# Performance work log

Measured on AMD Instinct MI355X. Metric: run time of the kernel, lower is better.

Reference implementation:

```python
import jax, jax.numpy as jnp
import numpy as np

D = 512      # d_model
H = 8        # num_heads
HD = D // H  # head_dim = 64
NI = 3       # num_inputs


def setup_inputs() -> dict:
    key = jax.random.key(0)
    ks = jax.random.split(key, 20)
    b, n, ni = 4, 8192, 4096
    s = 0.02
    inp = {
        "x": jax.random.normal(ks[0], (b, n, D), jnp.float32),
        "emb0": jax.random.normal(ks[1], (b, ni, D), jnp.float32),
        "emb1": jax.random.normal(ks[2], (b, ni, D), jnp.float32),
        "emb2": jax.random.normal(ks[3], (b, ni, D), jnp.float32),
        "Wq": jax.random.normal(ks[4], (D, D), jnp.float32) * s,
        "bq": jnp.zeros((D,), jnp.float32),
        "Wk": jax.random.normal(ks[5], (NI, D, D), jnp.float32) * s,
        "bk": jnp.zeros((NI, D), jnp.float32),
        "Wv": jax.random.normal(ks[6], (NI, D, D), jnp.float32) * s,
        "bv": jnp.zeros((NI, D), jnp.float32),
        "Wo": jax.random.normal(ks[7], (D, D), jnp.float32) * s,
        "bo": jnp.zeros((D,), jnp.float32),
        "mask0": jax.random.randint(ks[8], (b, ni), 0, 2).astype(bool),
        "mask1": jax.random.randint(ks[9], (b, ni), 0, 2).astype(bool),
        "mask2": jax.random.randint(ks[10], (b, ni), 0, 2).astype(bool),
    }
    return inp


def _heads(t, b):
    # [b, n, D] -> [b, H, n, HD]
    return t.reshape(b, -1, H, HD).transpose(0, 2, 1, 3)


def reference(x, emb0, emb1, emb2, Wq, bq, Wk, bk, Wv, bv, Wo, bo, mask0, mask1, mask2):
    b, n, _ = x.shape
    q = jax.nn.softmax(_heads(x @ Wq.T + bq, b), axis=-1)  # [b,H,n,HD]
    out = q
    for i, (emb, mask) in enumerate(((emb0, mask0), (emb1, mask1), (emb2, mask2))):
        k = jax.nn.softmax(_heads(emb @ Wk[i].T + bk[i], b), axis=-1)  # [b,H,ni,HD]
        v = _heads(emb @ Wv[i].T + bv[i], b)                            # [b,H,ni,HD]
        k = jnp.where(mask[:, None, :, None], k, 0.0)
        k_sum = k.sum(axis=2, keepdims=True)                            # [b,H,1,HD]
        d_inv = 1.0 / jnp.sum(q * k_sum, axis=-1, keepdims=True)        # [b,H,n,1]
        kv = jnp.einsum('bhsd,bhse->bhde', k, v)                        # [b,H,HD,HD]
        out = out + jnp.einsum('bhnd,bhde->bhne', q, kv) * d_inv
    out = out.transpose(0, 2, 1, 3).reshape(b, n, D) / NI
    return out @ Wo.T + bo
```

## Files before the change

kernel.cpp:

```cpp
#include <hip/hip_runtime.h>

#define D_MODEL 512
#define NH 8
#define HD_ 64
#define NUM_I 3
#define B_ 4
#define NSEQ 8192
#define SSEQ 4096

typedef __attribute__((ext_vector_type(8))) short short8;
typedef __attribute__((ext_vector_type(4))) float floatx4;

static constexpr size_t Q_OFF    = 0;
static constexpr size_t Q2_OFF   = 8388608;
static constexpr size_t KT_OFF   = 16777216;
static constexpr size_t VT_OFF   = 20971520;
static constexpr size_t WB_OFF   = 25165824;
static constexpr size_t KV_OFF   = 26214400;
static constexpr size_t KS_OFF   = 26607616;
static constexpr size_t KVB_OFF  = 26613760;
static constexpr size_t FLAG_OFF = 26712064;

__device__ __forceinline__ float bf2f(unsigned short u) {
    union { unsigned i; float f; } v; v.i = ((unsigned)u) << 16; return v.f;
}
__device__ __forceinline__ unsigned short f2bf(float f) {
    union { float f; unsigned i; } v; v.f = f;
    unsigned r = v.i + 0x7fffu + ((v.i >> 16) & 1u);
    return (unsigned short)(r >> 16);
}
__device__ __forceinline__ void gld16(const void* g, void* l) {
    __builtin_amdgcn_global_load_lds((const __attribute__((address_space(1))) void*)g,
                                     (__attribute__((address_space(3))) void*)l, 16, 0, 0);
}
__device__ __forceinline__ short8 cvt8(const float4& a, const float4& b) {
    short8 r;
    r[0] = (short)f2bf(a.x); r[1] = (short)f2bf(a.y);
    r[2] = (short)f2bf(a.z); r[3] = (short)f2bf(a.w);
    r[4] = (short)f2bf(b.x); r[5] = (short)f2bf(b.y);
    r[6] = (short)f2bf(b.z); r[7] = (short)f2bf(b.w);
    return r;
}

__global__ void mask_mode_kernel(const int* __restrict__ m, int* __restrict__ flag)
{
    __shared__ int any;
    if (threadIdx.x == 0) any = 0;
    __syncthreads();
    const unsigned v = (unsigned)m[threadIdx.x];
    if (v > 1u) atomicOr(&any, 1);
    __syncthreads();
    if (threadIdx.x == 0) *flag = any;
}

__global__ __launch_bounds__(256)
void f2bf_kernel(const float* __restrict__ in, unsigned short* __restrict__ out, int n8)
{
    const int i = blockIdx.x * 256 + threadIdx.x;
    if (i >= n8) return;
    const float4 a = ((const float4*)in)[2*i];
    const float4 b = ((const float4*)in)[2*i + 1];
    ((short8*)out)[i] = cvt8(a, b);
}

template<int EPI, int OUT, bool AFP32>
__global__ __launch_bounds__(256)
void proj2(const void* __restrict__ Av, const unsigned short* __restrict__ W,
           const float* __restrict__ bias, const int* __restrict__ mask,
           const int* __restrict__ maskmode, void* __restrict__ Cv)
{
    __shared__ short Ws[64 * 520];
    const int tid = threadIdx.x;
    const int wid = tid >> 6, lane = tid & 63;
    const int l15 = lane & 15, lq = lane >> 4;
    const int m0w = blockIdx.x * 256 + wid * 64;
    const int n0  = blockIdx.y * 64;

#pragma unroll
    for (int j = 0; j < 16; ++j) {
        const int row = wid * 16 + j;
        gld16(W + (size_t)(n0 + row) * D_MODEL + lane * 8, Ws + row * 520);
    }
    __syncthreads();

    floatx4 acc[4][4] = {};
    const float*          Af = (const float*)Av;
    const unsigned short* Ab = (const unsigned short*)Av;

    size_t abase[4];
#pragma unroll
    for (int mt = 0; mt < 4; ++mt)
        abase[mt] = (size_t)(m0w + mt * 16 + l15) * D_MODEL + lq * 8;

    short8 afc[4];
    if (AFP32) {
        float4 buf[2][4][2];
#pragma unroll
        for (int mt = 0; mt < 4; ++mt) {
            const float4* p0 = (const float4*)(Af + abase[mt]);
            buf[0][mt][0] = p0[0]; buf[0][mt][1] = p0[1];
            const float4* p1 = (const float4*)(Af + abase[mt] + 32);
            buf[1][mt][0] = p1[0]; buf[1][mt][1] = p1[1];
        }
#pragma unroll
        for (int mt = 0; mt < 4; ++mt) afc[mt] = cvt8(buf[0][mt][0], buf[0][mt][1]);
#pragma unroll
        for (int kk = 0; kk < 16; ++kk) {
            const int k0 = kk * 32;
            if (kk < 14) {
#pragma unroll
                for (int mt = 0; mt < 4; ++mt) {
                    const float4* p = (const float4*)(Af + abase[mt] + k0 + 64);
                    buf[kk & 1][mt][0] = p[0]; buf[kk & 1][mt][1] = p[1];
                }
            }
            short8 bfr[4];
#pragma unroll
            for (int nt = 0; nt < 4; ++nt)
                bfr[nt] = *(const short8*)&Ws[(nt * 16 + l15) * 520 + k0 + lq * 8];
#pragma unroll
            for (int mt = 0; mt < 4; ++mt)
#pragma unroll
                for (int nt = 0; nt < 4; ++nt)
                    acc[mt][nt] = __builtin_amdgcn_mfma_f32_16x16x32_bf16(afc[mt], bfr[nt], acc[mt][nt], 0, 0, 0);
            if (kk < 15) {
#pragma unroll
                for (int mt = 0; mt < 4; ++mt)
                    afc[mt] = cvt8(buf[(kk + 1) & 1][mt][0], buf[(kk + 1) & 1][mt][1]);
            }
        }
    } else {
        short8 buf[2][4];
#pragma unroll
        for (int mt = 0; mt < 4; ++mt) {
            buf[0][mt] = *(const short8*)(Ab + abase[mt]);
            buf[1][mt] = *(const short8*)(Ab + abase[mt] + 32);
        }
#pragma unroll
        for (int mt = 0; mt < 4; ++mt) afc[mt] = buf[0][mt];
#pragma unroll
        for (int kk = 0; kk < 16; ++kk) {
            const int k0 = kk * 32;
            if (kk < 14) {
#pragma unroll
                for (int mt = 0; mt < 4; ++mt)
                    buf[kk & 1][mt] = *(const short8*)(Ab + abase[mt] + k0 + 64);
            }
            short8 bfr[4];
#pragma unroll
            for (int nt = 0; nt < 4; ++nt)
                bfr[nt] = *(const short8*)&Ws[(nt * 16 + l15) * 520 + k0 + lq * 8];
#pragma unroll
            for (int mt = 0; mt < 4; ++mt)
#pragma unroll
                for (int nt = 0; nt < 4; ++nt)
                    acc[mt][nt] = __builtin_amdgcn_mfma_f32_16x16x32_bf16(afc[mt], bfr[nt], acc[mt][nt], 0, 0, 0);
            if (kk < 15) {
#pragma unroll
                for (int mt = 0; mt < 4; ++mt) afc[mt] = buf[(kk + 1) & 1][mt];
            }
        }
    }

    float bl[4];
#pragma unroll
    for (int nt = 0; nt < 4; ++nt) bl[nt] = bias[n0 + nt * 16 + l15];
#pragma unroll
    for (int mt = 0; mt < 4; ++mt)
#pragma unroll
        for (int nt = 0; nt < 4; ++nt)
#pragma unroll
            for (int r = 0; r < 4; ++r) acc[mt][nt][r] += bl[nt];

    if (EPI >= 1) {
#pragma unroll
        for (int mt = 0; mt < 4; ++mt)
#pragma unroll
            for (int r = 0; r < 4; ++r) {
                float mx = fmaxf(fmaxf(acc[mt][0][r], acc[mt][1][r]),
                                 fmaxf(acc[mt][2][r], acc[mt][3][r]));
#pragma unroll
                for (int off = 1; off < 16; off <<= 1) mx = fmaxf(mx, __shfl_xor(mx, off));
                float s = 0.f;
#pragma unroll
                for (int nt = 0; nt < 4; ++nt) {
                    const float e = __expf(acc[mt][nt][r] - mx);
                    acc[mt][nt][r] = e; s += e;
                }
#pragma unroll
                for (int off = 1; off < 16; off <<= 1) s += __shfl_xor(s, off);
                const float inv = 1.f / s;
#pragma unroll
                for (int nt = 0; nt < 4; ++nt) acc[mt][nt][r] *= inv;
            }
    }
    if (EPI == 2) {
        const int bytemode = *maskmode;
#pragma unroll
        for (int mt = 0; mt < 4; ++mt)
#pragma unroll
            for (int r = 0; r < 4; ++r) {
                const int grow = m0w + mt * 16 + lq * 4 + r;
                const bool keep = bytemode ? (((const unsigned char*)mask)[grow] != 0)
                                           : (mask[grow] != 0);
                if (!keep) {
#pragma unroll
                    for (int nt = 0; nt < 4; ++nt) acc[mt][nt][r] = 0.f;
                }
            }
    }

    if (OUT == 2) {
        __syncthreads();
        short* tw = Ws + wid * 4608;
#pragma unroll
        for (int mt = 0; mt < 4; ++mt)
#pragma unroll
            for (int nt = 0; nt < 4; ++nt) {
                ushort4 p;
                p.x = f2bf(acc[mt][nt][0]); p.y = f2bf(acc[mt][nt][1]);
                p.z = f2bf(acc[mt][nt][2]); p.w = f2bf(acc[mt][nt][3]);
                *(ushort4*)&tw[(nt * 16 + l15) * 72 + mt * 16 + lq * 4] = p;
            }
        __syncthreads();
        const int b_idx  = m0w >> 12;
        const int s_base = m0w & 4095;
        const int h = blockIdx.y;
        unsigned short* outp = (unsigned short*)Cv +
            ((size_t)(b_idx * NH + h) * 64 + lane) * SSEQ + s_base;
        const short* src = &tw[lane * 72];
#pragma unroll
        for (int sc = 0; sc < 8; ++sc)
            *(short8*)&outp[sc * 8] = *(const short8*)&src[sc * 8];
    } else {
#pragma unroll
        for (int mt = 0; mt < 4; ++mt)
#pragma unroll
            for (int r = 0; r < 4; ++r) {
                const size_t row = m0w + mt * 16 + lq * 4 + r;
#pragma unroll
                for (int nt = 0; nt < 4; ++nt) {
                    const int col = n0 + nt * 16 + l15;
                    if (OUT == 1)
                        ((unsigned short*)Cv)[row * D_MODEL + col] = f2bf(acc[mt][nt][r]);
                    else
                        ((float*)Cv)[row * D_MODEL + col] = acc[mt][nt][r];
                }
            }
    }
}

__global__ __launch_bounds__(256)
void kv_accum_mfma(const unsigned short* __restrict__ kT, const unsigned short* __restrict__ vT,
                   float* __restrict__ kv, float* __restrict__ ksum, int i_idx)
{
    const int chunk = blockIdx.x;
    const int h = blockIdx.y, b = blockIdx.z;
    __shared__ short As[2048];
    __shared__ short Bs[2048];
    const int tid = threadIdx.x;
    const int wid = tid >> 6, lane = tid & 63;
    const int wm  = wid & 1,  wn  = wid >> 1;
    const int l15 = lane & 15, lq = lane >> 4;

    const size_t base = (size_t)(b * NH + h) * 64 * SSEQ + chunk * 512;
    const int srow = tid & 63, ssub = tid >> 6;
    const unsigned short* Ag = vT + base + (size_t)srow * SSEQ + ssub * 8;
    const unsigned short* Bg = kT + base + (size_t)srow * SSEQ + ssub * 8;
    short* AsW = As + wid * 512;
    short* BsW = Bs + wid * 512;

    floatx4 acc[2][2] = {};
    floatx4 ks[2] = {};
    short8 ones;
#pragma unroll
    for (int j = 0; j < 8; ++j) ones[j] = (short)0x3F80;

    const int aoff = (wm*32 + l15)*8;
    const int boff = (wn*32 + l15)*8;

    for (int k0 = 0; k0 < 512; k0 += 32) {
        __syncthreads();
        gld16(Ag + k0, AsW);
        gld16(Bg + k0, BsW);
        __syncthreads();
        short8 af[2], bfr[2];
#pragma unroll
        for (int mt = 0; mt < 2; ++mt) af[mt]  = *(const short8*)&As[lq*512 + aoff + mt*128];
#pragma unroll
        for (int nt = 0; nt < 2; ++nt) bfr[nt] = *(const short8*)&Bs[lq*512 + boff + nt*128];
#pragma unroll
        for (int mt = 0; mt < 2; ++mt)
#pragma unroll
            for (int nt = 0; nt < 2; ++nt)
                acc[mt][nt] = __builtin_amdgcn_mfma_f32_16x16x32_bf16(af[mt], bfr[nt], acc[mt][nt], 0, 0, 0);
        if (wm == 0) {
#pragma unroll
            for (int nt = 0; nt < 2; ++nt)
                ks[nt] = __builtin_amdgcn_mfma_f32_16x16x32_bf16(ones, bfr[nt], ks[nt], 0, 0, 0);
        }
    }
    float* kvb = kv + (size_t)((i_idx*B_ + b)*NH + h) * 4096;
#pragma unroll
    for (int mt = 0; mt < 2; ++mt)
#pragma unroll
        for (int nt = 0; nt < 2; ++nt)
#pragma unroll
            for (int r = 0; r < 4; ++r) {
                const int e = wm*32 + mt*16 + lq*4 + r;
                const int d = wn*32 + nt*16 + l15;
                atomicAdd(&kvb[e*64 + d], acc[mt][nt][r]);
            }
    if (wm == 0 && lq == 0) {
        float* ksb = ksum + (size_t)((i_idx*B_ + b)*NH + h) * 64;
#pragma unroll
        for (int nt = 0; nt < 2; ++nt)
            atomicAdd(&ksb[wn*32 + nt*16 + l15], ks[nt][0]);
    }
}

__global__ __launch_bounds__(256)
void combine_mfma(const unsigned short* __restrict__ Q, const unsigned short* __restrict__ kvT,
                  const float* __restrict__ ksum, unsigned short* __restrict__ Qo)
{
    const int m0 = blockIdx.x * 128;
    const int h  = blockIdx.y;
    const int b  = m0 >> 13;
    __shared__ short qs[8192];
    __shared__ float skl[NUM_I][64];
    __shared__ float dinv[NUM_I][128];
    const int tid = threadIdx.x;
    const int wid = tid >> 6, lane = tid & 63;
    const int l15 = lane & 15, lq = lane >> 4;

    const unsigned short* Qbase = Q + (size_t)m0 * D_MODEL + h * 64;
#pragma unroll
    for (int j = 0; j < 4; ++j) {
        const int g = tid + j * 256;
        const int row = g & 127, c = g >> 7;
        gld16(Qbase + (size_t)row * D_MODEL + c * 8, qs + (size_t)(wid*64 + j*256) * 8);
    }
    if (tid < NUM_I * 64) {
        const int i = tid >> 6, d = tid & 63;
        skl[i][d] = ksum[(size_t)((i*B_ + b)*NH + h) * 64 + d];
    }
    __syncthreads();
    for (int it = tid; it < NUM_I * 128; it += 256) {
        const int i = it >> 7, row = it & 127;
        float s = 0.f;
#pragma unroll
        for (int d = 0; d < 64; ++d)
            s += bf2f((unsigned short)qs[(d >> 3)*1024 + row*8 + (d & 7)]) * skl[i][d];
        dinv[i][row] = 1.f / s;
    }
    __syncthreads();

    short8 af[2][2];
#pragma unroll
    for (int mt = 0; mt < 2; ++mt)
#pragma unroll
        for (int ks = 0; ks < 2; ++ks)
            af[mt][ks] = *(const short8*)&qs[(ks*4 + lq)*1024 + (wid*32 + mt*16 + l15)*8];

    floatx4 accO[2][4] = {};
    for (int i = 0; i < NUM_I; ++i) {
        const unsigned short* kvb = kvT + (size_t)((i*B_ + b)*NH + h) * 4096;
        short8 bfr[4][2];
#pragma unroll
        for (int nt = 0; nt < 4; ++nt)
#pragma unroll
            for (int ks = 0; ks < 2; ++ks)
                bfr[nt][ks] = *(const short8*)&kvb[(nt*16 + l15)*64 + ks*32 + lq*8];
#pragma unroll
        for (int mt = 0; mt < 2; ++mt)
#pragma unroll
            for (int nt = 0; nt < 4; ++nt) {
                floatx4 p = {};
                p = __builtin_amdgcn_mfma_f32_16x16x32_bf16(af[mt][0], bfr[nt][0], p, 0, 0, 0);
                p = __builtin_amdgcn_mfma_f32_16x16x32_bf16(af[mt][1], bfr[nt][1], p, 0, 0, 0);
#pragma unroll
                for (int r = 0; r < 4; ++r) {
                    const int row = wid*32 + mt*16 + lq*4 + r;
                    accO[mt][nt][r] += p[r] * dinv[i][row];
                }
            }
    }
    const float inv3 = 1.f / 3.f;
#pragma unroll
    for (int mt = 0; mt < 2; ++mt)
#pragma unroll
        for (int nt = 0; nt < 4; ++nt)
#pragma unroll
            for (int r = 0; r < 4; ++r) {
                const int row = wid*32 + mt*16 + lq*4 + r;
                const int col = nt*16 + l15;
                const float qv = bf2f((unsigned short)qs[(col >> 3)*1024 + row*8 + (col & 7)]);
                Qo[(size_t)(m0 + row) * D_MODEL + h*64 + col] = f2bf((qv + accO[mt][nt][r]) * inv3);
            }
}

extern "C" void kernel_launch(void* const* d_in, const int* in_sizes, int n_in,
                              void* d_out, int out_size, void* d_ws, size_t ws_size,
                              hipStream_t stream)
{
    const float* x      = (const float*)d_in[0];
    const float* emb[3] = {(const float*)d_in[1], (const float*)d_in[2], (const float*)d_in[3]};
    const float* Wq = (const float*)d_in[4];
    const float* bq = (const float*)d_in[5];
    const float* Wk = (const float*)d_in[6];
    const float* bk = (const float*)d_in[7];
    const float* Wv = (const float*)d_in[8];
    const float* bv = (const float*)d_in[9];
    const float* Wo = (const float*)d_in[10];
    const float* bo = (const float*)d_in[11];
    const int* mask[3] = {(const int*)d_in[12], (const int*)d_in[13], (const int*)d_in[14]};
    float* out = (float*)d_out;

    float* ws = (float*)d_ws;
    unsigned short* qb   = (unsigned short*)(ws + Q_OFF);
    unsigned short* q2b  = (unsigned short*)(ws + Q2_OFF);
    unsigned short* kT   = (unsigned short*)(ws + KT_OFF);
    unsigned short* vT   = (unsigned short*)(ws + VT_OFF);
    unsigned short* wb   = (unsigned short*)(ws + WB_OFF);
    unsigned short* wqb  = wb;
    unsigned short* wkb  = wb + 262144;
    unsigned short* wvb  = wb + 1048576;
    unsigned short* wob  = wb + 1835008;
    float* kv   = ws + KV_OFF;
    float* ksum = ws + KS_OFF;
    unsigned short* kvb16 = (unsigned short*)(ws + KVB_OFF);
    int*   flag = (int*)(ws + FLAG_OFF);

    mask_mode_kernel<<<1, 256, 0, stream>>>(mask[0], flag);
    hipMemsetAsync(kv, 0, (size_t)(NUM_I*B_*NH*HD_*HD_ + NUM_I*B_*NH*HD_) * sizeof(float), stream);

    f2bf_kernel<<<128, 256, 0, stream>>>(Wq, wqb, 32768);
    f2bf_kernel<<<384, 256, 0, stream>>>(Wk, wkb, 98304);
    f2bf_kernel<<<384, 256, 0, stream>>>(Wv, wvb, 98304);
    f2bf_kernel<<<128, 256, 0, stream>>>(Wo, wob, 32768);

    const dim3 gq(B_*NSEQ/256, NH);
    const dim3 gk(B_*SSEQ/256, NH);

    proj2<1, 1, true ><<<gq, 256, 0, stream>>>(x, wqb, bq, nullptr, nullptr, qb);
    for (int i = 0; i < NUM_I; ++i) {
        proj2<2, 2, true ><<<gk, 256, 0, stream>>>(emb[i], wkb + (size_t)i*262144,
                                                   bk + (size_t)i*D_MODEL, mask[i], flag, kT);
        proj2<0, 2, true ><<<gk, 256, 0, stream>>>(emb[i], wvb + (size_t)i*262144,
                                                   bv + (size_t)i*D_MODEL, nullptr, nullptr, vT);
        kv_accum_mfma<<<dim3(8, NH, B_), 256, 0, stream>>>(kT, vT, kv, ksum, i);
    }
    f2bf_kernel<<<192, 256, 0, stream>>>(kv, kvb16, 49152);
    combine_mfma<<<dim3(B_*NSEQ/128, NH), 256, 0, stream>>>(qb, kvb16, ksum, q2b);
    proj2<0, 0, false><<<gq, 256, 0, stream>>>(q2b, wob, bo, nullptr, nullptr, out);
}
```

Before: 679.7 us.

## Pre-convert activations to bf16 and restructure projection GEMM with swizzled LDS

Activations x and each embedding are converted to bf16 in separate passes, so the projection kernel reads bf16 A directly. The eight x-projection weight-tile loads for K and V each re-read fp32 emb, and that duplicate fp32 traffic should drop. The kernel now uses a 6-deep register prefetch of A, an XOR-swizzled unpadded LDS weight tile, and an occupancy hint of 2 blocks per SM. Epilogues for row-major outputs are staged through LDS for vectorized coalesced stores. The trade-off is extra conversion kernels and extra bf16 write/read traffic, plus a workspace layout reshuffle with aliased regions.

```diff
diff --git a/kernel.cpp b/kernel.cpp
--- a/kernel.cpp
+++ b/kernel.cpp
@@ -12,9 +12,11 @@
 typedef __attribute__((ext_vector_type(4))) float floatx4;
 
 static constexpr size_t Q_OFF    = 0;
+static constexpr size_t KT_OFF   = 8388608;
+static constexpr size_t VT_OFF   = 12582912;
 static constexpr size_t Q2_OFF   = 8388608;
-static constexpr size_t KT_OFF   = 16777216;
-static constexpr size_t VT_OFF   = 20971520;
+static constexpr size_t XB_OFF   = 16777216;
+static constexpr size_t EMBB_OFF = 16777216;
 static constexpr size_t WB_OFF   = 25165824;
 static constexpr size_t KV_OFF   = 26214400;
 static constexpr size_t KS_OFF   = 26607616;
@@ -63,13 +65,13 @@
     ((short8*)out)[i] = cvt8(a, b);
 }
 
-template<int EPI, int OUT, bool AFP32>
-__global__ __launch_bounds__(256)
-void proj2(const void* __restrict__ Av, const unsigned short* __restrict__ W,
+template<int EPI, int OUT>
+__global__ __launch_bounds__(256, 2)
+void proj3(const unsigned short* __restrict__ A, const unsigned short* __restrict__ W,
            const float* __restrict__ bias, const int* __restrict__ mask,
            const int* __restrict__ maskmode, void* __restrict__ Cv)
 {
-    __shared__ short Ws[64 * 520];
+    __shared__ __align__(16) short Ws[32768];
     const int tid = threadIdx.x;
     const int wid = tid >> 6, lane = tid & 63;
     const int l15 = lane & 15, lq = lane >> 4;
@@ -78,87 +80,43 @@
 
 #pragma unroll
     for (int j = 0; j < 16; ++j) {
-        const int row = wid * 16 + j;
-        gld16(W + (size_t)(n0 + row) * D_MODEL + lane * 8, Ws + row * 520);
+        const int col = wid * 16 + j;
+        gld16(W + (size_t)(n0 + col) * D_MODEL + ((lane ^ (col & 7)) << 3), Ws + col * 512);
     }
     __syncthreads();
 
     floatx4 acc[4][4] = {};
-    const float*          Af = (const float*)Av;
-    const unsigned short* Ab = (const unsigned short*)Av;
-
-    size_t abase[4];
+    const unsigned short* Arow[4];
 #pragma unroll
     for (int mt = 0; mt < 4; ++mt)
-        abase[mt] = (size_t)(m0w + mt * 16 + l15) * D_MODEL + lq * 8;
-
-    short8 afc[4];
-    if (AFP32) {
-        float4 buf[2][4][2];
-#pragma unroll
-        for (int mt = 0; mt < 4; ++mt) {
-            const float4* p0 = (const float4*)(Af + abase[mt]);
-            buf[0][mt][0] = p0[0]; buf[0][mt][1] = p0[1];
-            const float4* p1 = (const float4*)(Af + abase[mt] + 32);
-            buf[1][mt][0] = p1[0]; buf[1][mt][1] = p1[1];
-        }
-#pragma unroll
-        for (int mt = 0; mt < 4; ++mt) afc[mt] = cvt8(buf[0][mt][0], buf[0][mt][1]);
-#pragma unroll
-        for (int kk = 0; kk < 16; ++kk) {
-            const int k0 = kk * 32;
-            if (kk < 14) {
-#pragma unroll
-                for (int mt = 0; mt < 4; ++mt) {
-                    const float4* p = (const float4*)(Af + abase[mt] + k0 + 64);
-                    buf[kk & 1][mt][0] = p[0]; buf[kk & 1][mt][1] = p[1];
-                }
-            }
-            short8 bfr[4];
+        Arow[mt] = A + (size_t)(m0w + mt * 16 + l15) * D_MODEL + lq * 8;
+
+    short8 afb[6][4];
+#pragma unroll
+    for (int s = 0; s < 6; ++s)
+#pragma unroll
+        for (int mt = 0; mt < 4; ++mt)
+            afb[s][mt] = *(const short8*)(Arow[mt] + s * 32);
+
+    const int swz = l15 & 7;
+#pragma unroll
+    for (int ks = 0; ks < 16; ++ks) {
+        const int slot = ks % 6;
+        short8 bfr[4];
+#pragma unroll
+        for (int nt = 0; nt < 4; ++nt) {
+            const int kg = (ks * 4 + lq) ^ swz;
+            bfr[nt] = *(const short8*)&Ws[(nt * 16 + l15) * 512 + kg * 8];
+        }
+#pragma unroll
+        for (int mt = 0; mt < 4; ++mt)
 #pragma unroll
             for (int nt = 0; nt < 4; ++nt)
-                bfr[nt] = *(const short8*)&Ws[(nt * 16 + l15) * 520 + k0 + lq * 8];
+                acc[mt][nt] = __builtin_amdgcn_mfma_f32_16x16x32_bf16(afb[slot][mt], bfr[nt], acc[mt][nt], 0, 0, 0);
+        if (ks < 10) {
 #pragma unroll
             for (int mt = 0; mt < 4; ++mt)
-#pragma unroll
-                for (int nt = 0; nt < 4; ++nt)
-                    acc[mt][nt] = __builtin_amdgcn_mfma_f32_16x16x32_bf16(afc[mt], bfr[nt], acc[mt][nt], 0, 0, 0);
-            if (kk < 15) {
-#pragma unroll
-                for (int mt = 0; mt < 4; ++mt)
-                    afc[mt] = cvt8(buf[(kk + 1) & 1][mt][0], buf[(kk + 1) & 1][mt][1]);
-            }
-        }
-    } else {
-        short8 buf[2][4];
-#pragma unroll
-        for (int mt = 0; mt < 4; ++mt) {
-            buf[0][mt] = *(const short8*)(Ab + abase[mt]);
-            buf[1][mt] = *(const short8*)(Ab + abase[mt] + 32);
-        }
-#pragma unroll
-        for (int mt = 0; mt < 4; ++mt) afc[mt] = buf[0][mt];
-#pragma unroll
-        for (int kk = 0; kk < 16; ++kk) {
-            const int k0 = kk * 32;
-            if (kk < 14) {
-#pragma unroll
-                for (int mt = 0; mt < 4; ++mt)
-                    buf[kk & 1][mt] = *(const short8*)(Ab + abase[mt] + k0 + 64);
-            }
-            short8 bfr[4];
-#pragma unroll
-            for (int nt = 0; nt < 4; ++nt)
-                bfr[nt] = *(const short8*)&Ws[(nt * 16 + l15) * 520 + k0 + lq * 8];
-#pragma unroll
-            for (int mt = 0; mt < 4; ++mt)
-#pragma unroll
-                for (int nt = 0; nt < 4; ++nt)
-                    acc[mt][nt] = __builtin_amdgcn_mfma_f32_16x16x32_bf16(afc[mt], bfr[nt], acc[mt][nt], 0, 0, 0);
-            if (kk < 15) {
-#pragma unroll
-                for (int mt = 0; mt < 4; ++mt) afc[mt] = buf[(kk + 1) & 1][mt];
-            }
+                afb[slot][mt] = *(const short8*)(Arow[mt] + (ks + 6) * 32);
         }
     }
 
@@ -210,9 +168,9 @@
             }
     }
 
+    __syncthreads();
     if (OUT == 2) {
-        __syncthreads();
-        short* tw = Ws + wid * 4608;
+        short* tw = Ws + wid * 8192;
 #pragma unroll
         for (int mt = 0; mt < 4; ++mt)
 #pragma unroll
@@ -220,33 +178,61 @@
                 ushort4 p;
                 p.x = f2bf(acc[mt][nt][0]); p.y = f2bf(acc[mt][nt][1]);
                 p.z = f2bf(acc[mt][nt][2]); p.w = f2bf(acc[mt][nt][3]);
-                *(ushort4*)&tw[(nt * 16 + l15) * 72 + mt * 16 + lq * 4] = p;
+                *(ushort4*)&tw[mt * 1536 + (nt * 16 + l15) * 24 + lq * 4] = p;
             }
         __syncthreads();
         const int b_idx  = m0w >> 12;
         const int s_base = m0w & 4095;
-        const int h = blockIdx.y;
         unsigned short* outp = (unsigned short*)Cv +
-            ((size_t)(b_idx * NH + h) * 64 + lane) * SSEQ + s_base;
-        const short* src = &tw[lane * 72];
-#pragma unroll
-        for (int sc = 0; sc < 8; ++sc)
-            *(short8*)&outp[sc * 8] = *(const short8*)&src[sc * 8];
+            ((size_t)(b_idx * NH + blockIdx.y) * 64 + lane) * SSEQ + s_base;
+#pragma unroll
+        for (int mt = 0; mt < 4; ++mt) {
+            const short8 p0 = *(const short8*)&tw[mt * 1536 + lane * 24];
+            const short8 p1 = *(const short8*)&tw[mt * 1536 + lane * 24 + 8];
+            *(short8*)&outp[mt * 16]     = p0;
+            *(short8*)&outp[mt * 16 + 8] = p1;
+        }
+    } else if (OUT == 1) {
+        short* tw = Ws + wid * 8192;
+#pragma unroll
+        for (int mt = 0; mt < 4; ++mt)
+#pragma unroll
+            for (int nt = 0; nt < 4; ++nt)
+#pragma unroll
+                for (int r = 0; r < 4; ++r)
+                    tw[mt * 1024 + (lq * 4 + r) * 64 + nt * 16 + l15] = (short)f2bf(acc[mt][nt][r]);
+        __syncthreads();
+        const int sp = lane >> 2, ch = lane & 3;
+        unsigned short* Crow = (unsigned short*)Cv;
+#pragma unroll
+        for (int mt = 0; mt < 4; ++mt) {
+            const size_t row = m0w + mt * 16 + sp;
+            const short8 p0 = *(const short8*)&tw[mt * 1024 + sp * 64 + ch * 16];
+            const short8 p1 = *(const short8*)&tw[mt * 1024 + sp * 64 + ch * 16 + 8];
+            *(short8*)&Crow[row * D_MODEL + n0 + ch * 16]     = p0;
+            *(short8*)&Crow[row * D_MODEL + n0 + ch * 16 + 8] = p1;
+        }
     } else {
-#pragma unroll
-        for (int mt = 0; mt < 4; ++mt)
-#pragma unroll
-            for (int r = 0; r < 4; ++r) {
-                const size_t row = m0w + mt * 16 + lq * 4 + r;
-#pragma unroll
-                for (int nt = 0; nt < 4; ++nt) {
-                    const int col = n0 + nt * 16 + l15;
-                    if (OUT == 1)
-                        ((unsigned short*)Cv)[row * D_MODEL + col] = f2bf(acc[mt][nt][r]);
-                    else
-                        ((float*)Cv)[row * D_MODEL + col] = acc[mt][nt][r];
-                }
-            }
+        float* twf = (float*)(Ws + wid * 8192);
+#pragma unroll
+        for (int mt = 0; mt < 4; ++mt)
+#pragma unroll
+            for (int nt = 0; nt < 4; ++nt)
+#pragma unroll
+                for (int r = 0; r < 4; ++r)
+                    twf[mt * 1024 + (lq * 4 + r) * 64 + nt * 16 + l15] = acc[mt][nt][r];
+        __syncthreads();
+        const int sp = lane >> 2, ch = lane & 3;
+        float* Crow = (float*)Cv;
+#pragma unroll
+        for (int mt = 0; mt < 4; ++mt) {
+            const size_t row = m0w + mt * 16 + sp;
+#pragma unroll
+            for (int t = 0; t < 4; ++t) {
+                const float4 p = *(const float4*)&twf[mt * 1024 + sp * 64 + ch * 16 + t * 4];
+                *(float4*)&Crow[row * D_MODEL + n0 + ch * 16 + t * 4] = p;
+            }
+        }
     }
 }
 
@@ -418,9 +404,11 @@
 
     float* ws = (float*)d_ws;
     unsigned short* qb   = (unsigned short*)(ws + Q_OFF);
-    unsigned short* q2b  = (unsigned short*)(ws + Q2_OFF);
     unsigned short* kT   = (unsigned short*)(ws + KT_OFF);
     unsigned short* vT   = (unsigned short*)(ws + VT_OFF);
+    unsigned short* q2b  = (unsigned short*)(ws + Q2_OFF);
+    unsigned short* xb   = (unsigned short*)(ws + XB_OFF);
+    unsigned short* embb = (unsigned short*)(ws + EMBB_OFF);
     unsigned short* wb   = (unsigned short*)(ws + WB_OFF);
     unsigned short* wqb  = wb;
     unsigned short* wkb  = wb + 262144;
@@ -434,23 +422,25 @@
     mask_mode_kernel<<<1, 256, 0, stream>>>(mask[0], flag);
     hipMemsetAsync(kv, 0, (size_t)(NUM_I*B_*NH*HD_*HD_ + NUM_I*B_*NH*HD_) * sizeof(float), stream);
 
-    f2bf_kernel<<<128, 256, 0, stream>>>(Wq, wqb, 32768);
-    f2bf_kernel<<<384, 256, 0, stream>>>(Wk, wkb, 98304);
-    f2bf_kernel<<<384, 256, 0, stream>>>(Wv, wvb, 98304);
-    f2bf_kernel<<<128, 256, 0, stream>>>(Wo, wob, 32768);
+    f2bf_kernel<<<128,  256, 0, stream>>>(Wq, wqb, 32768);
+    f2bf_kernel<<<384,  256, 0, stream>>>(Wk, wkb, 98304);
+    f2bf_kernel<<<384,  256, 0, stream>>>(Wv, wvb, 98304);
+    f2bf_kernel<<<128,  256, 0, stream>>>(Wo, wob, 32768);
+    f2bf_kernel<<<8192, 256, 0, stream>>>(x,  xb,  2097152);
 
     const dim3 gq(B_*NSEQ/256, NH);
     const dim3 gk(B_*SSEQ/256, NH);
 
-    proj2<1, 1, true ><<<gq, 256, 0, stream>>>(x, wqb, bq, nullptr, nullptr, qb);
+    proj3<1, 1><<<gq, 256, 0, stream>>>(xb, wqb, bq, nullptr, nullptr, qb);
     for (int i = 0; i < NUM_I; ++i) {
-        proj2<2, 2, true ><<<gk, 256, 0, stream>>>(emb[i], wkb + (size_t)i*262144,
-                                                   bk + (size_t)i*D_MODEL, mask[i], flag, kT);
-        proj2<0, 2, true ><<<gk, 256, 0, stream>>>(emb[i], wvb + (size_t)i*262144,
-                                                   bv + (size_t)i*D_MODEL, nullptr, nullptr, vT);
+        f2bf_kernel<<<4096, 256, 0, stream>>>(emb[i], embb, 1048576);
+        proj3<2, 2><<<gk, 256, 0, stream>>>(embb, wkb + (size_t)i*262144,
+                                            bk + (size_t)i*D_MODEL, mask[i], flag, kT);
+        proj3<0, 2><<<gk, 256, 0, stream>>>(embb, wvb + (size_t)i*262144,
+                                            bv + (size_t)i*D_MODEL, nullptr, nullptr, vT);
         kv_accum_mfma<<<dim3(8, NH, B_), 256, 0, stream>>>(kT, vT, kv, ksum, i);
     }
     f2bf_kernel<<<192, 256, 0, stream>>>(kv, kvb16, 49152);
     combine_mfma<<<dim3(B_*NSEQ/128, NH), 256, 0, stream>>>(qb, kvb16, ksum, q2b);
-    proj2<0, 0, false><<<gq, 256, 0, stream>>>(q2b, wob, bo, nullptr, nullptr, out);
-}
+    proj3<0, 0><<<gq, 256, 0, stream>>>(q2b, wob, bo, nullptr, nullptr, out);
+}
```

Result: faster. 573.4 us (-15.6%).
